# Optimization experiments

Measured on AMD Instinct MI355X. Metric: run time of the kernel, lower is better.

Reference implementation:

```python
import itertools
import jax, jax.numpy as jnp
import numpy as np

GRID = 16384      # self.shape = (GRID,)
LAYERS = 8        # num_layers
SPAN = 2          # span = (2,)
K = 2 * SPAN + 1  # kernel size = 5 (ninputs)
NPOS = 2 ** K     # 32 possible boolean input combos
BATCH = 32
M = 4096          # x width; GRID % M == 0
STRIDE = GRID // M

# bitmask: all 2^K boolean input combinations, shape (NPOS, K)
_BITMASK = jnp.asarray(list(itertools.product(range(2), repeat=K)), dtype=jnp.float32)


def setup_inputs() -> dict:
    key = jax.random.key(0)
    k1, k2 = jax.random.split(key)
    x = jax.random.uniform(k1, (BATCH, M), dtype=jnp.float32)
    toggle_gates = jax.random.uniform(k2, (LAYERS, NPOS, GRID), dtype=jnp.float32)
    return {"x": x, "toggle_gates": toggle_gates}


def _convolve(state):
    # torch convolve(): offsets 0..K-1 via wrap-around roll, then spatial roll by
    # -SPAN to center the window -> neighbor n+i-SPAN (mod GRID) at kernel idx i.
    # jnp.roll(state, SPAN - i) gives out[:, n] = state[:, n + i - SPAN mod GRID].
    return jnp.stack([jnp.roll(state, SPAN - i, axis=1) for i in range(K)], axis=-1)  # (B, N, K)


def reference(x, toggle_gates):
    tw = jax.nn.sigmoid(toggle_gates)  # (L, NPOS, N)
    # embed(): scatter x evenly into the grid, rest is scratch (zeros)
    state = jnp.zeros((x.shape[0], GRID), dtype=x.dtype).at[:, ::STRIDE].set(x)

    def step(s, tw_layer):
        conv = _convolve(s)  # (B, N, K)
        # weight[c, b, n] = prod_i (1 - |bitmask[c, i] - conv[b, n, i]|)
        w = jnp.prod(1.0 - jnp.abs(_BITMASK[:, None, None, :] - conv[None]), axis=-1)  # (C, B, N)
        new = jnp.clip(jnp.einsum('cbn,cn->bn', w, tw_layer), 0.0, 1.0)
        return new, None

    state, _ = jax.lax.scan(step, state, tw)
    # forward returns state[slices] = state[:, ::STRIDE]
    return state[:, ::STRIDE]
```

## Files before the change

### kernel.cpp

```cpp
#include <hip/hip_runtime.h>

#define GRID_N 16384
#define NLAYERS 8
#define NPOS 32
#define BATCH 32
#define MW 4096
#define TILE 32
#define HALO 16
#define WBUF 64
#define ROWP 36

__global__ __launch_bounds__(512, 4) void ASIC_44186623541335_kernel(
    const float* __restrict__ x,
    const float* __restrict__ tg,
    float* __restrict__ out)
{
    __shared__ __align__(16) float st[WBUF][ROWP];
    __shared__ __align__(16) float twl[4][WBUF][ROWP];

    const int tid = threadIdx.x;
    const int tx  = tid & 63;
    const int ty  = tid >> 6;
    const int c0  = 4 * ty;
    const int start = blockIdx.x * TILE;
    const int gcol  = (start - HALO + tx) & (GRID_N - 1);

    float pf[16];
    #pragma unroll
    for (int l4 = 0; l4 < 4; ++l4)
        #pragma unroll
        for (int k = 0; k < 4; ++k)
            pf[l4 * 4 + k] = tg[((size_t)l4 * NPOS + c0 + k) * GRID_N + gcol];

    for (int f = tid; f < WBUF * BATCH; f += 512) {
        const int b = f >> 6;
        const int j = f & 63;
        const int g = (start - HALO + j) & (GRID_N - 1);
        st[j][b] = ((g & 3) == 0) ? x[b * MW + (g >> 2)] : 0.0f;
    }

    #pragma unroll
    for (int l4 = 0; l4 < 4; ++l4) {
        float4 sg;
        sg.x = __builtin_amdgcn_rcpf(1.0f + __expf(-pf[l4 * 4 + 0]));
        sg.y = __builtin_amdgcn_rcpf(1.0f + __expf(-pf[l4 * 4 + 1]));
        sg.z = __builtin_amdgcn_rcpf(1.0f + __expf(-pf[l4 * 4 + 2]));
        sg.w = __builtin_amdgcn_rcpf(1.0f + __expf(-pf[l4 * 4 + 3]));
        *(float4*)&twl[l4][tx][c0] = sg;
    }
    #pragma unroll
    for (int l4 = 0; l4 < 4; ++l4)
        #pragma unroll
        for (int k = 0; k < 4; ++k)
            pf[l4 * 4 + k] = tg[((size_t)(4 + l4) * NPOS + c0 + k) * GRID_N + gcol];
    __syncthreads();

    for (int l = 0; l < NLAYERS; ++l) {
        const int h     = 2 * (NLAYERS - 1 - l);
        const int ncols = TILE + 2 * h;
        const int j     = (HALO - h) + tx;

        if (tx < ncols) {
            float tw[32];
            #pragma unroll
            for (int k = 0; k < 8; ++k) {
                const float4 q = *(const float4*)&twl[l & 3][j][4 * k];
                tw[4 * k]     = q.x; tw[4 * k + 1] = q.y;
                tw[4 * k + 2] = q.z; tw[4 * k + 3] = q.w;
            }

            float4 res;
            #pragma unroll
            for (int p = 0; p < 2; ++p) {
                const float2 S0 = *(const float2*)&st[j - 2][c0 + 2 * p];
                const float2 S1 = *(const float2*)&st[j - 1][c0 + 2 * p];
                const float2 S2 = *(const float2*)&st[j    ][c0 + 2 * p];
                const float2 S3 = *(const float2*)&st[j + 1][c0 + 2 * p];
                const float2 S4 = *(const float2*)&st[j + 2][c0 + 2 * p];

                float ua[16], ub[16];
                #pragma unroll
                for (int r = 0; r < 16; ++r) {
                    const float d = tw[16 + r] - tw[r];
                    ua[r] = fmaf(S0.x, d, tw[r]);
                    ub[r] = fmaf(S0.y, d, tw[r]);
                }
                #pragma unroll
                for (int r = 0; r < 8; ++r) {
                    const float da = ua[8 + r] - ua[r], db = ub[8 + r] - ub[r];
                    ua[r] = fmaf(S1.x, da, ua[r]);
                    ub[r] = fmaf(S1.y, db, ub[r]);
                }
                #pragma unroll
                for (int r = 0; r < 4; ++r) {
                    const float da = ua[4 + r] - ua[r], db = ub[4 + r] - ub[r];
                    ua[r] = fmaf(S2.x, da, ua[r]);
                    ub[r] = fmaf(S2.y, db, ub[r]);
                }
                #pragma unroll
                for (int r = 0; r < 2; ++r) {
                    const float da = ua[2 + r] - ua[r], db = ub[2 + r] - ub[r];
                    ua[r] = fmaf(S3.x, da, ua[r]);
                    ub[r] = fmaf(S3.y, db, ub[r]);
                }
                const float da = ua[1] - ua[0], db = ub[1] - ub[0];
                float ra = fmaf(S4.x, da, ua[0]);
                float rb = fmaf(S4.y, db, ub[0]);
                ra = fminf(fmaxf(ra, 0.0f), 1.0f);
                rb = fminf(fmaxf(rb, 0.0f), 1.0f);
                if (p) { res.z = ra; res.w = rb; } else { res.x = ra; res.y = rb; }
            }
            *(float4*)&st[j][c0] = res;
        }
        __builtin_amdgcn_wave_barrier();

        if (l == 3) {
            __syncthreads();
            #pragma unroll
            for (int l4 = 0; l4 < 4; ++l4) {
                float4 sg;
                sg.x = __builtin_amdgcn_rcpf(1.0f + __expf(-pf[l4 * 4 + 0]));
                sg.y = __builtin_amdgcn_rcpf(1.0f + __expf(-pf[l4 * 4 + 1]));
                sg.z = __builtin_amdgcn_rcpf(1.0f + __expf(-pf[l4 * 4 + 2]));
                sg.w = __builtin_amdgcn_rcpf(1.0f + __expf(-pf[l4 * 4 + 3]));
                *(float4*)&twl[l4][tx][c0] = sg;
            }
            __syncthreads();
        }
    }

    __syncthreads();
    if (tid < 256) {
        const int c4 = tid & 7;
        const int b  = tid >> 3;
        out[b * MW + (start >> 2) + c4] = st[HALO + 4 * c4][b];
    }
}

extern "C" void kernel_launch(void* const* d_in, const int* in_sizes, int n_in,
                              void* d_out, int out_size, void* d_ws, size_t ws_size,
                              hipStream_t stream) {
    const float* x  = (const float*)d_in[0];
    const float* tg = (const float*)d_in[1];
    float* out = (float*)d_out;
    ASIC_44186623541335_kernel<<<GRID_N / TILE, 512, 0, stream>>>(x, tg, out);
}
```

Baseline: 82.11 us.

## Halve block size, give each thread 8 batches, use packed f2 FMAs

Cuts the block from 512 to 256 threads, so each thread now handles 8 batch rows instead of 4. The 16 weight differences (tw[16+r]-tw[r]) are computed once per layer and reused across four batch pairs instead of being recomputed per pair. The interpolation chain uses 2-wide vector FMAs that can map to packed fp32 instructions. The aim is more register-level reuse of the per-column weights and fewer instructions, at the cost of higher register pressure, lower occupancy per block (launch bounds 256,2), and a doubled per-thread prefetch array.

```diff
diff --git a/kernel.cpp b/kernel.cpp
--- a/kernel.cpp
+++ b/kernel.cpp
@@ -10,7 +10,9 @@
 #define WBUF 64
 #define ROWP 36
 
-__global__ __launch_bounds__(512, 4) void ASIC_44186623541335_kernel(
+typedef float f2 __attribute__((ext_vector_type(2)));
+
+__global__ __launch_bounds__(256, 2) void ASIC_44186623541335_kernel(
     const float* __restrict__ x,
     const float* __restrict__ tg,
     float* __restrict__ out)
@@ -21,18 +23,18 @@
     const int tid = threadIdx.x;
     const int tx  = tid & 63;
     const int ty  = tid >> 6;
-    const int c0  = 4 * ty;
+    const int c0  = 8 * ty;
     const int start = blockIdx.x * TILE;
     const int gcol  = (start - HALO + tx) & (GRID_N - 1);
 
-    float pf[16];
+    float pf[32];
     #pragma unroll
     for (int l4 = 0; l4 < 4; ++l4)
         #pragma unroll
-        for (int k = 0; k < 4; ++k)
-            pf[l4 * 4 + k] = tg[((size_t)l4 * NPOS + c0 + k) * GRID_N + gcol];
+        for (int k = 0; k < 8; ++k)
+            pf[l4 * 8 + k] = tg[((size_t)l4 * NPOS + c0 + k) * GRID_N + gcol];
 
-    for (int f = tid; f < WBUF * BATCH; f += 512) {
+    for (int f = tid; f < WBUF * BATCH; f += 256) {
         const int b = f >> 6;
         const int j = f & 63;
         const int g = (start - HALO + j) & (GRID_N - 1);
@@ -41,18 +43,21 @@
 
     #pragma unroll
     for (int l4 = 0; l4 < 4; ++l4) {
-        float4 sg;
-        sg.x = __builtin_amdgcn_rcpf(1.0f + __expf(-pf[l4 * 4 + 0]));
-        sg.y = __builtin_amdgcn_rcpf(1.0f + __expf(-pf[l4 * 4 + 1]));
-        sg.z = __builtin_amdgcn_rcpf(1.0f + __expf(-pf[l4 * 4 + 2]));
-        sg.w = __builtin_amdgcn_rcpf(1.0f + __expf(-pf[l4 * 4 + 3]));
-        *(float4*)&twl[l4][tx][c0] = sg;
+        #pragma unroll
+        for (int h4 = 0; h4 < 2; ++h4) {
+            float4 sg;
+            sg.x = __builtin_amdgcn_rcpf(1.0f + __expf(-pf[l4 * 8 + 4 * h4 + 0]));
+            sg.y = __builtin_amdgcn_rcpf(1.0f + __expf(-pf[l4 * 8 + 4 * h4 + 1]));
+            sg.z = __builtin_amdgcn_rcpf(1.0f + __expf(-pf[l4 * 8 + 4 * h4 + 2]));
+            sg.w = __builtin_amdgcn_rcpf(1.0f + __expf(-pf[l4 * 8 + 4 * h4 + 3]));
+            *(float4*)&twl[l4][tx][c0 + 4 * h4] = sg;
+        }
     }
     #pragma unroll
     for (int l4 = 0; l4 < 4; ++l4)
         #pragma unroll
-        for (int k = 0; k < 4; ++k)
-            pf[l4 * 4 + k] = tg[((size_t)(4 + l4) * NPOS + c0 + k) * GRID_N + gcol];
+        for (int k = 0; k < 8; ++k)
+            pf[l4 * 8 + k] = tg[((size_t)(4 + l4) * NPOS + c0 + k) * GRID_N + gcol];
     __syncthreads();
 
     for (int l = 0; l < NLAYERS; ++l) {
@@ -68,49 +73,47 @@
                 tw[4 * k]     = q.x; tw[4 * k + 1] = q.y;
                 tw[4 * k + 2] = q.z; tw[4 * k + 3] = q.w;
             }
+            float d0[16];
+            #pragma unroll
+            for (int r = 0; r < 16; ++r) d0[r] = tw[16 + r] - tw[r];
 
-            float4 res;
+            float4 A[5][2];
             #pragma unroll
-            for (int p = 0; p < 2; ++p) {
-                const float2 S0 = *(const float2*)&st[j - 2][c0 + 2 * p];
-                const float2 S1 = *(const float2*)&st[j - 1][c0 + 2 * p];
-                const float2 S2 = *(const float2*)&st[j    ][c0 + 2 * p];
-                const float2 S3 = *(const float2*)&st[j + 1][c0 + 2 * p];
-                const float2 S4 = *(const float2*)&st[j + 2][c0 + 2 * p];
+            for (int o = 0; o < 5; ++o) {
+                A[o][0] = *(const float4*)&st[j - 2 + o][c0];
+                A[o][1] = *(const float4*)&st[j - 2 + o][c0 + 4];
+            }
 
-                float ua[16], ub[16];
+            float4 res[2];
+            #pragma unroll
+            for (int q = 0; q < 4; ++q) {
+                const int hi = q >> 1, lo = (q & 1) * 2;
+                const f2 s0 = { ((const float*)&A[0][hi])[lo], ((const float*)&A[0][hi])[lo + 1] };
+                const f2 s1 = { ((const float*)&A[1][hi])[lo], ((const float*)&A[1][hi])[lo + 1] };
+                const f2 s2 = { ((const float*)&A[2][hi])[lo], ((const float*)&A[2][hi])[lo + 1] };
+                const f2 s3 = { ((const float*)&A[3][hi])[lo], ((const float*)&A[3][hi])[lo + 1] };
+                const f2 s4 = { ((const float*)&A[4][hi])[lo], ((const float*)&A[4][hi])[lo + 1] };
+
+                f2 u[16];
                 #pragma unroll
-                for (int r = 0; r < 16; ++r) {
-                    const float d = tw[16 + r] - tw[r];
-                    ua[r] = fmaf(S0.x, d, tw[r]);
-                    ub[r] = fmaf(S0.y, d, tw[r]);
-                }
+                for (int r = 0; r < 16; ++r)
+                    u[r] = __builtin_elementwise_fma(s0, (f2)d0[r], (f2)tw[r]);
                 #pragma unroll
-                for (int r = 0; r < 8; ++r) {
-                    const float da = ua[8 + r] - ua[r], db = ub[8 + r] - ub[r];
-                    ua[r] = fmaf(S1.x, da, ua[r]);
-                    ub[r] = fmaf(S1.y, db, ub[r]);
-                }
+                for (int r = 0; r < 8; ++r)
+                    u[r] = __builtin_elementwise_fma(s1, u[8 + r] - u[r], u[r]);
                 #pragma unroll
-                for (int r = 0; r < 4; ++r) {
-                    const float da = ua[4 + r] - ua[r], db = ub[4 + r] - ub[r];
-                    ua[r] = fmaf(S2.x, da, ua[r]);
-                    ub[r] = fmaf(S2.y, db, ub[r]);
-                }
+                for (int r = 0; r < 4; ++r)
+                    u[r] = __builtin_elementwise_fma(s2, u[4 + r] - u[r], u[r]);
                 #pragma unroll
-                for (int r = 0; r < 2; ++r) {
-                    const float da = ua[2 + r] - ua[r], db = ub[2 + r] - ub[r];
-                    ua[r] = fmaf(S3.x, da, ua[r]);
-                    ub[r] = fmaf(S3.y, db, ub[r]);
-                }
-                const float da = ua[1] - ua[0], db = ub[1] - ub[0];
-                float ra = fmaf(S4.x, da, ua[0]);
-                float rb = fmaf(S4.y, db, ub[0]);
-                ra = fminf(fmaxf(ra, 0.0f), 1.0f);
-                rb = fminf(fmaxf(rb, 0.0f), 1.0f);
-                if (p) { res.z = ra; res.w = rb; } else { res.x = ra; res.y = rb; }
+                for (int r = 0; r < 2; ++r)
+                    u[r] = __builtin_elementwise_fma(s3, u[2 + r] - u[r], u[r]);
+                f2 rv = __builtin_elementwise_fma(s4, u[1] - u[0], u[0]);
+                rv = __builtin_elementwise_min(__builtin_elementwise_max(rv, (f2)0.0f), (f2)1.0f);
+                ((float*)&res[hi])[lo]     = rv.x;
+                ((float*)&res[hi])[lo + 1] = rv.y;
             }
-            *(float4*)&st[j][c0] = res;
+            *(float4*)&st[j][c0]     = res[0];
+            *(float4*)&st[j][c0 + 4] = res[1];
         }
         __builtin_amdgcn_wave_barrier();
 
@@ -118,19 +121,22 @@
             __syncthreads();
             #pragma unroll
             for (int l4 = 0; l4 < 4; ++l4) {
-                float4 sg;
-                sg.x = __builtin_amdgcn_rcpf(1.0f + __expf(-pf[l4 * 4 + 0]));
-                sg.y = __builtin_amdgcn_rcpf(1.0f + __expf(-pf[l4 * 4 + 1]));
-                sg.z = __builtin_amdgcn_rcpf(1.0f + __expf(-pf[l4 * 4 + 2]));
-                sg.w = __builtin_amdgcn_rcpf(1.0f + __expf(-pf[l4 * 4 + 3]));
-                *(float4*)&twl[l4][tx][c0] = sg;
+                #pragma unroll
+                for (int h4 = 0; h4 < 2; ++h4) {
+                    float4 sg;
+                    sg.x = __builtin_amdgcn_rcpf(1.0f + __expf(-pf[l4 * 8 + 4 * h4 + 0]));
+                    sg.y = __builtin_amdgcn_rcpf(1.0f + __expf(-pf[l4 * 8 + 4 * h4 + 1]));
+                    sg.z = __builtin_amdgcn_rcpf(1.0f + __expf(-pf[l4 * 8 + 4 * h4 + 2]));
+                    sg.w = __builtin_amdgcn_rcpf(1.0f + __expf(-pf[l4 * 8 + 4 * h4 + 3]));
+                    *(float4*)&twl[l4][tx][c0 + 4 * h4] = sg;
+                }
             }
             __syncthreads();
         }
     }
 
     __syncthreads();
-    if (tid < 256) {
+    {
         const int c4 = tid & 7;
         const int b  = tid >> 3;
         out[b * MW + (start >> 2) + c4] = st[HALO + 4 * c4][b];
@@ -143,5 +149,5 @@
     const float* x  = (const float*)d_in[0];
     const float* tg = (const float*)d_in[1];
     float* out = (float*)d_out;
-    ASIC_44186623541335_kernel<<<GRID_N / TILE, 512, 0, stream>>>(x, tg, out);
+    ASIC_44186623541335_kernel<<<GRID_N / TILE, 256, 0, stream>>>(x, tg, out);
 }
```

After: 82.68 us. Within noise of the previous version (+0.7%).
